# Kernel optimization log

Hardware: AMD Instinct MI355X
Metric: run time of the kernel (lower is better)

## Reference

```python
import jax, jax.numpy as jnp
import numpy as np

DIM = 512
HEADS = 8
DIM_HEAD = 64
BLOCKS = 6
EXCHANGES = 3
EPS = 1.1920929e-07  # torch.finfo(float32).eps used by RMSNorm(eps=None)


def _rmsnorm(x, w):
    return x * jax.lax.rsqrt(jnp.mean(x * x, axis=-1, keepdims=True) + EPS) * w


def _attention(x, ctx, nw, wq, wkv, wo):
    # x: [B, i, d] queries; ctx: [B, j, d] context (NOT normalized, as in original)
    B = x.shape[0]
    xn = _rmsnorm(x, nw)
    q = jnp.einsum('bid,ed->bie', xn, wq)
    kv = jnp.einsum('bjd,ed->bje', ctx, wkv)
    k, v = jnp.split(kv, 2, axis=-1)
    heads = lambda t: t.reshape(B, t.shape[1], HEADS, DIM_HEAD).transpose(0, 2, 1, 3)
    q, k, v = heads(q), heads(k), heads(v)
    sim = jnp.einsum('bhid,bhjd->bhij', q, k)  # NOTE: original never applies self.scale
    attn = jax.nn.softmax(sim, axis=-1)
    out = jnp.einsum('bhij,bhjd->bhid', attn, v)
    out = out.transpose(0, 2, 1, 3).reshape(B, -1, HEADS * DIM_HEAD)
    return jnp.einsum('bie,de->bid', out, wo)


def _feedforward(x, nw, kw, kb, vw, vb):
    q = _rmsnorm(x, nw)
    h = jnp.einsum('...d,ed->...e', q, kw) + kb
    sim, gates = jnp.split(h, 2, axis=-1)
    h = sim * jax.nn.gelu(gates, approximate=False)  # F.gelu default = exact erf
    return jnp.einsum('...e,de->...d', h, vw) + vb


def _forward(tokens, attn_norm_w, attn_wq, attn_wkv, attn_wo,
             ff_norm_w, ff_keys_w, ff_keys_b, ff_values_w, ff_values_b,
             res_norm_w, res_wq, res_wkv, res_wo):
    b, n, d = tokens.shape
    tokens = jnp.broadcast_to(tokens[None], (BLOCKS, b, n, d))
    messages = [tokens]
    for _ in range(EXCHANGES):
        flat = tokens.reshape(BLOCKS * b, n, d)
        attended = _attention(flat, flat, attn_norm_w, attn_wq, attn_wkv, attn_wo)
        attended = attended.reshape(BLOCKS, b, n, d)
        retrieved = _feedforward(tokens, ff_norm_w, ff_keys_w, ff_keys_b, ff_values_w, ff_values_b)
        messages += [attended, retrieved]
        packed = jnp.concatenate(messages, axis=0)           # [M, b, n, d]
        M = packed.shape[0]
        # einops: repeat 'm b n d -> (b blocks) n m d'
        ctx = jnp.broadcast_to(packed.transpose(1, 2, 0, 3)[:, None], (b, BLOCKS, n, M, d))
        ctx = ctx.reshape(b * BLOCKS * n, M, d)
        # queries packed '(blocks b) n d' then '* n d' -> [blocks*b*n, 1, d]
        q = tokens.reshape(BLOCKS * b * n, 1, d)
        pooled = _attention(q, ctx, res_norm_w, res_wq, res_wkv, res_wo)
        tokens = pooled.reshape(BLOCKS, b, n, d)
    return tokens


def setup_inputs() -> dict:
    key = jax.random.key(0)
    ks = jax.random.split(key, 12)
    b, n, d = 2, 256, DIM
    di = HEADS * DIM_HEAD
    dff = int(d * 4.0 * 2 / 3)
    s = lambda k, shp, fan: (jax.random.normal(k, shp, jnp.float32) / np.sqrt(fan)).astype(jnp.float32)
    return {
        'tokens': jax.random.normal(ks[0], (b, n, d), jnp.float32),
        'attn_norm_w': 1.0 + 0.05 * jax.random.normal(ks[1], (d,), jnp.float32),
        'attn_wq': s(ks[2], (di, d), d),
        'attn_wkv': s(ks[3], (2 * di, d), d),
        'attn_wo': s(ks[4], (d, di), di),
        'ff_norm_w': 1.0 + 0.05 * jax.random.normal(ks[5], (d,), jnp.float32),
        'ff_keys_w': s(ks[6], (2 * dff, d), d),
        'ff_keys_b': 0.01 * jax.random.normal(ks[7], (2 * dff,), jnp.float32),
        'ff_values_w': s(ks[8], (d, dff), dff),
        'ff_values_b': 0.01 * jax.random.normal(ks[9], (d,), jnp.float32),
        'res_norm_w': 1.0 + 0.05 * jax.random.normal(ks[10], (d,), jnp.float32),
        'res_wq': s(ks[11], (di, d), d),
        'res_wkv': s(jax.random.fold_in(key, 100), (2 * di, d), d),
        'res_wo': s(jax.random.fold_in(key, 101), (d, di), di),
    }


def reference(tokens, attn_norm_w, attn_wq, attn_wkv, attn_wo,
              ff_norm_w, ff_keys_w, ff_keys_b, ff_values_w, ff_values_b,
              res_norm_w, res_wq, res_wkv, res_wo):
    return _forward(tokens, attn_norm_w, attn_wq, attn_wkv, attn_wo,
                    ff_norm_w, ff_keys_w, ff_keys_b, ff_values_w, ff_values_b,
                    res_norm_w, res_wq, res_wkv, res_wo)
```

## Files before the change

### kernel.cpp

```cpp
#include <hip/hip_runtime.h>
#include <math.h>

#define Dm   512
#define Nn_  256
#define Bv   2
#define NTD  1024
#define NH   8
#define DH   64
#define DFF  1365
#define DFF2 2730
#define KFF  1408
#define NFF  2816
#define NMD  14
#define EPSR 1.1920929e-07f


typedef _Float16 h16;
typedef h16  v8h  __attribute__((ext_vector_type(8)));
typedef float v4f __attribute__((ext_vector_type(4)));

__device__ inline h16 f2h(float v) { return (h16)v; }

__device__ inline void glds16(const void* g, void* l) {
    __builtin_amdgcn_global_load_lds((const __attribute__((address_space(1))) void*)g,
                                     (__attribute__((address_space(3))) void*)l, 16, 0, 0);
}

struct GDesc {
    const h16* A;
    const h16* W;
    const float* bias;
    float* C;
    h16* Cbf;
    long Apl, Wpl, bfpl;
    int lda, ldw, ldc, Nd, mbase, K, mode, nbx;
};

template <int BM>
__global__ __launch_bounds__(256) void mega_gemm(GDesc d0, GDesc d1, GDesc d2,
                                                 int n0, int n01)
{
    constexpr int MI = BM / 32;
    constexpr int ASEG = BM / 16;
    constexpr int NSEG = 2 * ASEG + 16;
    constexpr int BUF = 2 * BM * 32 + 2 * 4096;
    constexpr int AH = 0, AL = BM * 32, WH = 2 * BM * 32, WL = 2 * BM * 32 + 4096;
    __shared__ h16 lds[2 * BUF];

    GDesc d; int lb = blockIdx.x;
    if (lb < n0) d = d0;
    else if (lb < n01) { d = d1; lb -= n0; }
    else { d = d2; lb -= n01; }
    const int bx = lb % d.nbx;
    const int by = lb / d.nbx;

    const int tid = threadIdx.x;
    const int wid = tid >> 6;
    const int lane = tid & 63;
    const int wm = wid >> 1, wn = wid & 1;
    const int row16 = lane & 15, quad = lane >> 4;
    const long i0 = (long)bx * BM;
    const long j0 = (long)by * 128;
    const int l4 = lane >> 2;
    const int l2s = ((lane & 3) ^ (l4 & 3)) * 8;
    const int ksw = (quad ^ (row16 & 3)) * 8;

    auto stage = [&](int k0, h16* buf) {
        #pragma unroll
        for (int s = 0; s < NSEG / 4; ++s) {
            const int sg = wid * (NSEG / 4) + s;
            const h16* src;
            int dst;
            if (sg < ASEG) {
                src = d.A + (i0 + sg * 16 + l4) * (long)d.lda + k0 + l2s;
                dst = AH + sg * 512;
            } else if (sg < 2 * ASEG) {
                const int r = sg - ASEG;
                src = d.A + d.Apl + (i0 + r * 16 + l4) * (long)d.lda + k0 + l2s;
                dst = AL + r * 512;
            } else if (sg < 2 * ASEG + 8) {
                const int r = sg - 2 * ASEG;
                src = d.W + (j0 + r * 16 + l4) * (long)d.ldw + k0 + l2s;
                dst = WH + r * 512;
            } else {
                const int r = sg - 2 * ASEG - 8;
                src = d.W + d.Wpl + (j0 + r * 16 + l4) * (long)d.ldw + k0 + l2s;
                dst = WL + r * 512;
            }
            glds16(src, &buf[dst]);
        }
    };

    v4f acc[MI][4];
    #pragma unroll
    for (int a = 0; a < MI; ++a)
        #pragma unroll
        for (int b = 0; b < 4; ++b) acc[a][b] = (v4f){0.f, 0.f, 0.f, 0.f};

    stage(0, lds);
    int cur = 0;
    for (int k0 = 0; k0 < d.K; k0 += 32) {
        __syncthreads();
        h16* cbuf = &lds[cur * BUF];
        if (k0 + 32 < d.K) stage(k0 + 32, &lds[(cur ^ 1) * BUF]);

        v8h af[MI], al[MI];
        #pragma unroll
        for (int mi = 0; mi < MI; ++mi) {
            const int aoff = (wm * (BM / 2) + mi * 16 + row16) * 32 + ksw;
            af[mi] = *(const v8h*)&cbuf[AH + aoff];
            al[mi] = *(const v8h*)&cbuf[AL + aoff];
        }
        #pragma unroll
        for (int nj = 0; nj < 4; ++nj) {
            const int boff = (wn * 64 + nj * 16 + row16) * 32 + ksw;
            v8h bh = *(const v8h*)&cbuf[WH + boff];
            v8h bl = *(const v8h*)&cbuf[WL + boff];
            #pragma unroll
            for (int mi = 0; mi < MI; ++mi) {
                acc[mi][nj] = __builtin_amdgcn_mfma_f32_16x16x32_f16(af[mi], bh, acc[mi][nj], 0, 0, 0);
                acc[mi][nj] = __builtin_amdgcn_mfma_f32_16x16x32_f16(af[mi], bl, acc[mi][nj], 0, 0, 0);
                acc[mi][nj] = __builtin_amdgcn_mfma_f32_16x16x32_f16(al[mi], bh, acc[mi][nj], 0, 0, 0);
            }
        }
        cur ^= 1;
    }

    #pragma unroll
    for (int nj = 0; nj < 4; ++nj) {
        const int col = (int)j0 + wn * 64 + nj * 16 + row16;
        if (col < d.Nd) {
            const float bv = d.bias ? d.bias[col] : 0.f;
            #pragma unroll
            for (int mi = 0; mi < MI; ++mi) {
                #pragma unroll
                for (int r = 0; r < 4; ++r) {
                    const long row = i0 + wm * (BM / 2) + mi * 16 + quad * 4 + r;
                    const float v = acc[mi][nj][r] + bv;
                    if (d.mode == 0) {
                        d.C[row * (long)d.ldc + col] = v;
                    } else if (d.mode == 1) {
                        const long idx = row * (long)d.ldc + col;
                        const h16 hi = f2h(v);
                        d.Cbf[idx] = hi; d.Cbf[idx + d.bfpl] = f2h(v - (float)hi);
                    } else if (d.mode == 2) {
                        const long idx = row * (long)d.ldc + col;
                        d.C[idx] = v;
                        const h16 hi = f2h(v);
                        d.Cbf[idx] = hi; d.Cbf[idx + d.bfpl] = f2h(v - (float)hi);
                    } else if (d.mode == 3) {
                        const int srel = (int)(row >> 10);
                        const int rr = (int)row & 1023;
                        const int md = (d.mbase + srel) * 2 + (rr >> 9);
                        const long orow = (long)(((rr >> 8) & 1) * 256 + (rr & 255)) * NMD + md;
                        d.C[orow * 1024 + col] = v;
                    } else if (d.mode == 4) {
                        const h16 hi = f2h(v);
                        const h16 lo = f2h(v - (float)hi);
                        if (col < 512) {
                            const long idx = row * 512 + col;
                            d.Cbf[idx] = hi; d.Cbf[idx + d.bfpl] = lo;
                        } else {
                            const int c = col - 512;
                            const int bh_ = ((int)(row >> 8)) * 8 + (c >> 6);
                            const long idx = (((long)bh_ * 64 + (c & 63)) << 8) + (row & 255);
                            h16* vtp = (h16*)d.C;
                            vtp[idx] = hi; vtp[idx + d.bfpl] = lo;
                        }
                    } else {
                        const int g = (int)(row >> 9), bb = ((int)row >> 8) & 1, nn = (int)row & 255;
                        #pragma unroll
                        for (int rep = 0; rep < 3; ++rep) {
                            const long orow = (long)(((g * 3 + rep) * 2 + bb) * 256 + nn);
                            d.C[orow * (long)d.ldc + col] = v;
                        }
                    }
                }
            }
        }
    }
}

__global__ void cvt_hilo(const float* __restrict__ x, int Ms, int Ks, int Kp,
                         h16* __restrict__ y, long plane, int total)
{
    const int idx = blockIdx.x * 256 + threadIdx.x;
    if (idx >= total) return;
    const int row = idx / Kp;
    const int col = idx - row * Kp;
    const float v = (row < Ms && col < Ks) ? x[(long)row * Ks + col] : 0.f;
    const h16 hi = f2h(v);
    y[idx] = hi;
    y[idx + plane] = f2h(v - (float)hi);
}

__global__ __launch_bounds__(256) void rmsnorm3_bf(
    const float* __restrict__ x,
    const float* __restrict__ w0, const float* __restrict__ w1,
    const float* __restrict__ w2,
    h16* __restrict__ y0, h16* __restrict__ y1,
    h16* __restrict__ y2, long plane)
{
    const int r = blockIdx.x;
    const float* xr = x + (long)r * Dm;
    const int t = threadIdx.x;
    const float a = xr[t];
    const float b = xr[t + 256];
    float ss = a * a + b * b;
    #pragma unroll
    for (int off = 32; off > 0; off >>= 1) ss += __shfl_xor(ss, off, 64);
    __shared__ float w4[4];
    if ((t & 63) == 0) w4[t >> 6] = ss;
    __syncthreads();
    const float rs = rsqrtf((w4[0] + w4[1] + w4[2] + w4[3]) * (1.f / 512.f) + EPSR);
    const float na = a * rs, nb = b * rs;
    const long ia = (long)r * Dm + t, ib = ia + 256;
    h16 h;
    float v;
    v = na * w0[t];       h = f2h(v); y0[ia] = h; y0[ia + plane] = f2h(v - (float)h);
    v = nb * w0[t + 256]; h = f2h(v); y0[ib] = h; y0[ib + plane] = f2h(v - (float)h);
    v = na * w1[t];       h = f2h(v); y1[ia] = h; y1[ia + plane] = f2h(v - (float)h);
    v = nb * w1[t + 256]; h = f2h(v); y1[ib] = h; y1[ib + plane] = f2h(v - (float)h);
    v = na * w2[t];       h = f2h(v); y2[ia] = h; y2[ia + plane] = f2h(v - (float)h);
    v = nb * w2[t + 256]; h = f2h(v); y2[ib] = h; y2[ib + plane] = f2h(v - (float)h);
}

__global__ __launch_bounds__(256) void glu_gelu_bf(
    const float* __restrict__ h, h16* __restrict__ y, long plane)
{
    const int r = blockIdx.x;
    const float* row = h + (long)r * NFF;
    for (int c = threadIdx.x; c < KFF; c += 256) {
        float v = 0.f;
        if (c < DFF) {
            const float sim = row[c];
            const float g = row[c + DFF];
            v = sim * (0.5f * g * (1.f + erff(g * 0.70710678118654752440f)));
        }
        const long idx = (long)r * KFF + c;
        const h16 hi = f2h(v);
        y[idx] = hi;
        y[idx + plane] = f2h(v - (float)hi);
    }
}

__global__ __launch_bounds__(256) void attn_self_mfma(
    const h16* __restrict__ qhl, const h16* __restrict__ khl,
    const h16* __restrict__ vtb, long pl, h16* __restrict__ outbf)
{
    __shared__ h16 kh[4096], kl[4096], vh[4096], vl[4096];
    __shared__ h16 pH[4 * 1024], pL[4 * 1024];

    const int bat = blockIdx.x >> 5;
    const int head = (blockIdx.x >> 2) & 7;
    const int qc = blockIdx.x & 3;
    const int t = threadIdx.x;
    const int w = t >> 6, lane = t & 63;
    const int row16 = lane & 15, quad = lane >> 4;

    v8h qh[2], ql[2];
    {
        const long qrow = (long)bat * 256 + qc * 64 + w * 16 + row16;
        const h16* qp = qhl + qrow * 512 + head * 64 + quad * 8;
        qh[0] = *(const v8h*)qp;        qh[1] = *(const v8h*)(qp + 32);
        ql[0] = *(const v8h*)(qp + pl); ql[1] = *(const v8h*)(qp + pl + 32);
    }

    v4f O[4];
    #pragma unroll
    for (int i = 0; i < 4; ++i) O[i] = (v4f){0.f, 0.f, 0.f, 0.f};
    float m[4] = {-1e30f, -1e30f, -1e30f, -1e30f};
    float l[4] = {0.f, 0.f, 0.f, 0.f};

    const int sj = t >> 3;
    const int sc = t & 7;
    const long kbase = ((long)bat * 256) * 512 + head * 64;
    const long vbase = ((long)(bat * 8 + head) * 64) << 8;

    for (int jc = 0; jc < 256; jc += 64) {
        __syncthreads();
        #pragma unroll
        for (int rep = 0; rep < 2; ++rep) {
            const int row = sj + rep * 32;
            const int dsw = row * 64 + ((sc ^ (row & 7)) * 8);
            const h16* ks = khl + kbase + (long)(jc + row) * 512 + sc * 8;
            const h16* vs = vtb + vbase + ((long)row << 8) + jc + sc * 8;
            *(v8h*)&kh[dsw] = *(const v8h*)ks;
            *(v8h*)&kl[dsw] = *(const v8h*)(ks + pl);
            *(v8h*)&vh[dsw] = *(const v8h*)vs;
            *(v8h*)&vl[dsw] = *(const v8h*)(vs + pl);
        }
        __syncthreads();

        v4f S[4];
        #pragma unroll
        for (int i = 0; i < 4; ++i) S[i] = (v4f){0.f, 0.f, 0.f, 0.f};
        #pragma unroll
        for (int kk = 0; kk < 2; ++kk) {
            #pragma unroll
            for (int tile = 0; tile < 4; ++tile) {
                const int off = (tile * 16 + row16) * 64 + (((kk * 4 + quad) ^ (row16 & 7)) * 8);
                v8h bh = *(const v8h*)&kh[off];
                v8h bl = *(const v8h*)&kl[off];
                S[tile] = __builtin_amdgcn_mfma_f32_16x16x32_f16(qh[kk], bh, S[tile], 0, 0, 0);
                S[tile] = __builtin_amdgcn_mfma_f32_16x16x32_f16(qh[kk], bl, S[tile], 0, 0, 0);
                S[tile] = __builtin_amdgcn_mfma_f32_16x16x32_f16(ql[kk], bh, S[tile], 0, 0, 0);
            }
        }

        float mc[4], sums[4], alpha[4];
        #pragma unroll
        for (int r = 0; r < 4; ++r) {
            float v = fmaxf(fmaxf(S[0][r], S[1][r]), fmaxf(S[2][r], S[3][r]));
            v = fmaxf(v, __shfl_xor(v, 1, 64));
            v = fmaxf(v, __shfl_xor(v, 2, 64));
            v = fmaxf(v, __shfl_xor(v, 4, 64));
            v = fmaxf(v, __shfl_xor(v, 8, 64));
            mc[r] = v;
        }
        #pragma unroll
        for (int r = 0; r < 4; ++r) {
            const float mn = fmaxf(m[r], mc[r]);
            alpha[r] = __expf(m[r] - mn);
            m[r] = mn;
            sums[r] = 0.f;
        }
        #pragma unroll
        for (int tile = 0; tile < 4; ++tile) {
            #pragma unroll
            for (int r = 0; r < 4; ++r) {
                const float p = __expf(S[tile][r] - m[r]);
                S[tile][r] = p;
                sums[r] += p;
            }
        }
        #pragma unroll
        for (int r = 0; r < 4; ++r) {
            float v = sums[r];
            v += __shfl_xor(v, 1, 64);
            v += __shfl_xor(v, 2, 64);
            v += __shfl_xor(v, 4, 64);
            v += __shfl_xor(v, 8, 64);
            l[r] = l[r] * alpha[r] + v;
        }
        #pragma unroll
        for (int tile = 0; tile < 4; ++tile)
            #pragma unroll
            for (int r = 0; r < 4; ++r) O[tile][r] *= alpha[r];

        #pragma unroll
        for (int tile = 0; tile < 4; ++tile) {
            const int chunkcol = tile * 2 + (row16 >> 3);
            #pragma unroll
            for (int r = 0; r < 4; ++r) {
                const int prow = quad * 4 + r;
                const int addr = w * 1024 + prow * 64 +
                                 ((chunkcol ^ (prow & 7)) * 8) + (row16 & 7);
                const float p = S[tile][r];
                const h16 hi = f2h(p);
                pH[addr] = hi;
                pL[addr] = f2h(p - (float)hi);
            }
        }

        #pragma unroll
        for (int kk = 0; kk < 2; ++kk) {
            const int poff = w * 1024 + row16 * 64 + (((kk * 4 + quad) ^ (row16 & 7)) * 8);
            v8h pa = *(const v8h*)&pH[poff];
            v8h pb = *(const v8h*)&pL[poff];
            #pragma unroll
            for (int tile = 0; tile < 4; ++tile) {
                const int off = (tile * 16 + row16) * 64 + (((kk * 4 + quad) ^ (row16 & 7)) * 8);
                v8h vbh = *(const v8h*)&vh[off];
                v8h vbl = *(const v8h*)&vl[off];
                O[tile] = __builtin_amdgcn_mfma_f32_16x16x32_f16(pa, vbh, O[tile], 0, 0, 0);
                O[tile] = __builtin_amdgcn_mfma_f32_16x16x32_f16(pa, vbl, O[tile], 0, 0, 0);
                O[tile] = __builtin_amdgcn_mfma_f32_16x16x32_f16(pb, vbh, O[tile], 0, 0, 0);
            }
        }
    }

    #pragma unroll
    for (int tile = 0; tile < 4; ++tile) {
        const int dim = tile * 16 + row16;
        #pragma unroll
        for (int r = 0; r < 4; ++r) {
            const long grow = (long)bat * 256 + qc * 64 + w * 16 + quad * 4 + r;
            const float v = O[tile][r] / l[r];
            const long idx = grow * 512 + head * 64 + dim;
            const h16 hi = f2h(v);
            outbf[idx] = hi;
            outbf[idx + pl] = f2h(v - (float)hi);
        }
    }
}

template <int M>
__global__ __launch_bounds__(128) void attn_pool_kernel(
    const float* __restrict__ qb, const float* __restrict__ kvc3,
    h16* __restrict__ outbf, long plane)
{
    const int rb = blockIdx.x >> 3;
    const int h = blockIdx.x & 7;
    __shared__ float k_lds[M * 66];
    __shared__ float v_lds[M * 66];
    __shared__ float q_lds[2 * 64];
    __shared__ float p_lds[2 * 64];
    const int t = threadIdx.x;
    const int g = rb >> 8, nn = rb & 255;

    for (int idx = t; idx < M * 64; idx += 128) {
        const int m = idx >> 6, d = idx & 63;
        const long base = ((long)rb * NMD + m) * 1024 + h * DH + d;
        k_lds[m * 66 + d] = kvc3[base];
        v_lds[m * 66 + d] = kvc3[base + 512];
    }
    {
        const int w = t >> 6, dd = t & 63;
        const long iq = (long)(g * 2 + w) * 256 + nn;
        q_lds[t] = qb[iq * Dm + h * DH + dd];
    }
    __syncthreads();

    const int w = t >> 6;
    const int lane = t & 63;
    float s = -1e30f;
    if (lane < M) {
        s = 0.f;
        const float* kr = &k_lds[lane * 66];
        const float* qr = &q_lds[w * 64];
        #pragma unroll
        for (int dd = 0; dd < 64; dd += 2) {
            s = fmaf(qr[dd], kr[dd], s);
            s = fmaf(qr[dd + 1], kr[dd + 1], s);
        }
    }
    float mx = s;
    #pragma unroll
    for (int off = 32; off > 0; off >>= 1) mx = fmaxf(mx, __shfl_xor(mx, off, 64));
    const float p = __expf(s - mx);
    float l = p;
    #pragma unroll
    for (int off = 32; off > 0; off >>= 1) l += __shfl_xor(l, off, 64);
    p_lds[w * 64 + lane] = p / l;

    float o = 0.f;
    const float* pr = &p_lds[w * 64];
    #pragma unroll
    for (int m = 0; m < M; ++m)
        o = fmaf(pr[m], v_lds[m * 66 + lane], o);

    const long iq = (long)(g * 2 + w) * 256 + nn;
    const long oidx = iq * Dm + h * DH + lane;
    const h16 hi = f2h(o);
    outbf[oidx] = hi;
    outbf[oidx + plane] = f2h(o - (float)hi);
}

__global__ void replicate_kernel(const float* __restrict__ src,
                                 float* __restrict__ tokens,
                                 h16* __restrict__ tokbf, long tpl,
                                 h16* __restrict__ msg0, long mpl)
{
    const int idx = blockIdx.x * blockDim.x + threadIdx.x;
    if (idx >= NTD * Dm) return;
    const float v = src[idx & (Bv * Nn_ * Dm - 1)];
    tokens[idx] = v;
    const h16 hi = f2h(v);
    const h16 lo = f2h(v - (float)hi);
    tokbf[idx] = hi; tokbf[idx + tpl] = lo;
    msg0[idx] = hi; msg0[idx + mpl] = lo;
}

extern "C" void kernel_launch(void* const* d_in, const int* in_sizes, int n_in,
                              void* d_out, int out_size, void* d_ws, size_t ws_size,
                              hipStream_t stream)
{
    const float* tok_in       = (const float*)d_in[0];
    const float* attn_norm_w  = (const float*)d_in[1];
    const float* attn_wq      = (const float*)d_in[2];
    const float* attn_wkv     = (const float*)d_in[3];
    const float* attn_wo      = (const float*)d_in[4];
    const float* ff_norm_w    = (const float*)d_in[5];
    const float* ff_keys_w    = (const float*)d_in[6];
    const float* ff_keys_b    = (const float*)d_in[7];
    const float* ff_values_w  = (const float*)d_in[8];
    const float* ff_values_b  = (const float*)d_in[9];
    const float* res_norm_w   = (const float*)d_in[10];
    const float* res_wq       = (const float*)d_in[11];
    const float* res_wkv      = (const float*)d_in[12];
    const float* res_wo       = (const float*)d_in[13];

    float* ws = (float*)d_ws;
    float* kvc3   = ws;
    float* tokens = kvc3 + 512L * NMD * 1024;
    float* qbuf   = tokens + (long)NTD * Dm;
    float* hbuf   = qbuf + (long)NTD * Dm;

    h16* us = (h16*)(hbuf + (long)NTD * NFF);
    const long apl = (long)NTD * Dm;
    const long mpl = 7L * NTD * Dm;
    const long hpl = (long)NTD * KFF;
    const long vtpl = (long)NTD * Dm;
    const long w1 = 512L * 512, w2 = 1024L * 512, w3 = (long)NFF * 512, w4 = 512L * KFF;
    h16* msgs_bf = us; us += 2 * mpl;
    h16* tokbf   = us; us += 2 * apl;
    h16* xa      = us; us += 2 * apl;
    h16* xf      = us; us += 2 * apl;
    h16* xr      = us; us += 2 * apl;
    h16* abf     = us; us += 2 * apl;
    h16* hbf     = us; us += 2 * hpl;
    h16* qhl     = us; us += 2 * apl;
    h16* khl     = us; us += 2 * apl;
    h16* vtb     = us; us += 2 * vtpl;
    h16* wqb  = us; us += 2 * w1;
    h16* wkvb = us; us += 2 * w2;
    h16* wob  = us; us += 2 * w1;
    h16* fkb  = us; us += 2 * w3;
    h16* fvb  = us; us += 2 * w4;
    h16* rqb  = us; us += 2 * w1;
    h16* rkvb = us; us += 2 * w2;
    h16* rob  = us; us += 2 * w1;

    auto cvtw = [&](const float* src, int Ms, int Ks, int Kp, int Mpad,
                    h16* dst, long pl) {
        const int tot = Mpad * Kp;
        cvt_hilo<<<(tot + 255) / 256, 256, 0, stream>>>(src, Ms, Ks, Kp, dst, pl, tot);
    };
    cvtw(attn_wq,     512,  512,  512, 512,  wqb,  w1);
    cvtw(attn_wkv,    1024, 512,  512, 1024, wkvb, w2);
    cvtw(attn_wo,     512,  512,  512, 512,  wob,  w1);
    cvtw(ff_keys_w,   DFF2, 512,  512, NFF,  fkb,  w3);
    cvtw(ff_values_w, 512,  DFF,  KFF, 512,  fvb,  w4);
    cvtw(res_wq,      512,  512,  512, 512,  rqb,  w1);
    cvtw(res_wkv,    1024,  512,  512, 1024, rkvb, w2);
    cvtw(res_wo,      512,  512,  512, 512,  rob,  w1);

    replicate_kernel<<<(NTD * Dm + 255) / 256, 256, 0, stream>>>(
        tok_in, tokens, tokbf, apl, msgs_bf, mpl);

    auto mk = [](const h16* A, long Apl, int lda,
                 const h16* W, long Wpl, int ldw,
                 const float* bias, float* C, int ldc, int Nd,
                 h16* Cbf, long bfpl, int mbase, int K,
                 int mode, int nbx) -> GDesc {
        GDesc d;
        d.A = A; d.Apl = Apl; d.lda = lda;
        d.W = W; d.Wpl = Wpl; d.ldw = ldw;
        d.bias = bias; d.C = C; d.ldc = ldc; d.Nd = Nd;
        d.Cbf = Cbf; d.bfpl = bfpl; d.mbase = mbase; d.K = K;
        d.mode = mode; d.nbx = nbx;
        return d;
    };

    for (int e = 0; e < 3; ++e) {
        rmsnorm3_bf<<<NTD, 256, 0, stream>>>(tokens, attn_norm_w, ff_norm_w, res_norm_w,
                                             xa, xf, xr, apl);
        {
            GDesc dwq  = mk(xa,    apl, 512, wqb,  w1, 512, nullptr,   nullptr, 512, 512,
                            qhl, apl, 0, 512, 1, 16);
            GDesc dwkv = mk(tokbf, apl, 512, wkvb, w2, 512, nullptr,   (float*)vtb, 1024, 1024,
                            khl, apl, 0, 512, 4, 16);
            GDesc dffk = mk(xf,    apl, 512, fkb,  w3, 512, ff_keys_b, hbuf,  NFF,  DFF2,
                            nullptr, 0, 0, 512, 0, 16);
            mega_gemm<64><<<544, 256, 0, stream>>>(dwq, dwkv, dffk, 64, 192);
        }
        attn_self_mfma<<<4 * NH * 4, 256, 0, stream>>>(qhl, khl, vtb, apl, abf);
        glu_gelu_bf<<<NTD, 256, 0, stream>>>(hbuf, hbf, hpl);
        {
            GDesc dwo  = mk(abf, apl, 512,  wob, w1, 512,  nullptr,     nullptr, 512, 512,
                            msgs_bf + (1 + 2 * e) * (long)NTD * Dm, mpl, 0, 512, 1, 16);
            GDesc dffv = mk(hbf, hpl, KFF,  fvb, w4, KFF,  ff_values_b, nullptr, 512, 512,
                            msgs_bf + (2 + 2 * e) * (long)NTD * Dm, mpl, 0, KFF, 1, 16);
            GDesc drq  = mk(xr, apl, 512, rqb, w1, 512, nullptr, qbuf, 512, 512,
                            nullptr, 0, 0, 512, 0, 16);
            mega_gemm<64><<<192, 256, 0, stream>>>(dwo, dffv, drq, 64, 128);
        }
        {
            const int s0 = (e == 0) ? 0 : (1 + 2 * e);
            const int ns = (e == 0) ? 3 : 2;
            GDesc drkv = mk(msgs_bf + (long)s0 * NTD * Dm, mpl, 512, rkvb, w2, 512,
                            nullptr, kvc3, 1024, 1024, nullptr, 0, s0, 512, 3, ns * 16);
            const int nb = ns * 16 * 8;
            mega_gemm<64><<<nb, 256, 0, stream>>>(drkv, drkv, drkv, nb, nb);
        }
        if (e == 0)      attn_pool_kernel<6><<<512 * NH, 128, 0, stream>>>(qbuf, kvc3, abf, apl);
        else if (e == 1) attn_pool_kernel<10><<<512 * NH, 128, 0, stream>>>(qbuf, kvc3, abf, apl);
        else             attn_pool_kernel<14><<<512 * NH, 128, 0, stream>>>(qbuf, kvc3, abf, apl);
        {
            if (e < 2) {
                GDesc dro = mk(abf, apl, 512, rob, w1, 512, nullptr, tokens, 512, 512,
                               tokbf, apl, 0, 512, 2, 16);
                mega_gemm<64><<<64, 256, 0, stream>>>(dro, dro, dro, 64, 64);
            } else {
                GDesc dro = mk(abf, apl, 512, rob, w1, 512, nullptr, (float*)d_out, 512, 512,
                               nullptr, 0, 0, 512, 5, 16);
                mega_gemm<64><<<64, 256, 0, stream>>>(dro, dro, dro, 64, 64);
            }
        }
    }
}
```

Baseline: 522.4 us.

## Fold output projections into residual KV weights and fuse attention with GLU

Precomputes the products of res_wkv with attn_wo and ff_values_w, plus a folded bias, once per call. The KV projections of the attended and retrieved messages can then be computed straight from the attention output and the GLU activations, which drops the message hi/lo buffers and the separate KV GEMM launch. The self-attention and GLU-GELU kernels are merged into one launch, mega_gemm takes a fourth descriptor so more GEMMs share a launch, and the final projection uses BM=32 tiles for more blocks. In exchange there is a per-call weight-folding GEMM, a larger inner K (1408) on the FFN path, and an extra rounding step from the precomposed weights.

```diff
diff --git a/kernel.cpp b/kernel.cpp
--- a/kernel.cpp
+++ b/kernel.cpp
@@ -14,7 +14,6 @@
 #define NMD  14
 #define EPSR 1.1920929e-07f
 
-
 typedef _Float16 h16;
 typedef h16  v8h  __attribute__((ext_vector_type(8)));
 typedef float v4f __attribute__((ext_vector_type(4)));
@@ -37,8 +36,8 @@
 };
 
 template <int BM>
-__global__ __launch_bounds__(256) void mega_gemm(GDesc d0, GDesc d1, GDesc d2,
-                                                 int n0, int n01)
+__global__ __launch_bounds__(256) void mega_gemm(GDesc d0, GDesc d1, GDesc d2, GDesc d3,
+                                                 int n0, int n01, int n012)
 {
     constexpr int MI = BM / 32;
     constexpr int ASEG = BM / 16;
@@ -50,7 +49,8 @@
     GDesc d; int lb = blockIdx.x;
     if (lb < n0) d = d0;
     else if (lb < n01) { d = d1; lb -= n0; }
-    else { d = d2; lb -= n01; }
+    else if (lb < n012) { d = d2; lb -= n01; }
+    else { d = d3; lb -= n012; }
     const int bx = lb % d.nbx;
     const int by = lb / d.nbx;
 
@@ -149,9 +149,8 @@
                         const h16 hi = f2h(v);
                         d.Cbf[idx] = hi; d.Cbf[idx + d.bfpl] = f2h(v - (float)hi);
                     } else if (d.mode == 3) {
-                        const int srel = (int)(row >> 10);
                         const int rr = (int)row & 1023;
-                        const int md = (d.mbase + srel) * 2 + (rr >> 9);
+                        const int md = d.mbase * 2 + (rr >> 9);
                         const long orow = (long)(((rr >> 8) & 1) * 256 + (rr & 255)) * NMD + md;
                         d.C[orow * 1024 + col] = v;
                     } else if (d.mode == 4) {
@@ -194,6 +193,30 @@
     y[idx + plane] = f2h(v - (float)hi);
 }
 
+__global__ void cvt_hilo_T(const float* __restrict__ x, int R, int C,
+                           h16* __restrict__ y, long plane, int total)
+{
+    const int idx = blockIdx.x * 256 + threadIdx.x;
+    if (idx >= total) return;
+    const int row = idx / R;
+    const int col = idx - row * R;
+    const float v = (row < C) ? x[(long)col * C + row] : 0.f;
+    const h16 hi = f2h(v);
+    y[idx] = hi;
+    y[idx + plane] = f2h(v - (float)hi);
+}
+
+__global__ void fold_bias(const float* __restrict__ wkv, const float* __restrict__ b,
+                          float* __restrict__ out)
+{
+    const int n = blockIdx.x * 256 + threadIdx.x;
+    if (n >= 1024) return;
+    float s = 0.f;
+    const float* row = wkv + (long)n * 512;
+    for (int d2 = 0; d2 < 512; ++d2) s = fmaf(row[d2], b[d2], s);
+    out[n] = s;
+}
+
 __global__ __launch_bounds__(256) void rmsnorm3_bf(
     const float* __restrict__ x,
     const float* __restrict__ w0, const float* __restrict__ w1,
@@ -225,29 +248,29 @@
     v = nb * w2[t + 256]; h = f2h(v); y2[ib] = h; y2[ib + plane] = f2h(v - (float)h);
 }
 
-__global__ __launch_bounds__(256) void glu_gelu_bf(
-    const float* __restrict__ h, h16* __restrict__ y, long plane)
-{
-    const int r = blockIdx.x;
-    const float* row = h + (long)r * NFF;
-    for (int c = threadIdx.x; c < KFF; c += 256) {
-        float v = 0.f;
-        if (c < DFF) {
-            const float sim = row[c];
-            const float g = row[c + DFF];
-            v = sim * (0.5f * g * (1.f + erff(g * 0.70710678118654752440f)));
-        }
-        const long idx = (long)r * KFF + c;
-        const h16 hi = f2h(v);
-        y[idx] = hi;
-        y[idx + plane] = f2h(v - (float)hi);
-    }
-}
-
-__global__ __launch_bounds__(256) void attn_self_mfma(
+__global__ __launch_bounds__(256) void attn_glu(
     const h16* __restrict__ qhl, const h16* __restrict__ khl,
-    const h16* __restrict__ vtb, long pl, h16* __restrict__ outbf)
-{
+    const h16* __restrict__ vtb, long pl, h16* __restrict__ outbf,
+    const float* __restrict__ hbuf, h16* __restrict__ hbf, long hpl)
+{
+    if (blockIdx.x >= 128) {
+        const int r = blockIdx.x - 128;
+        const float* row = hbuf + (long)r * NFF;
+        for (int c = threadIdx.x; c < KFF; c += 256) {
+            float v = 0.f;
+            if (c < DFF) {
+                const float sim = row[c];
+                const float g = row[c + DFF];
+                v = sim * (0.5f * g * (1.f + erff(g * 0.70710678118654752440f)));
+            }
+            const long idx = (long)r * KFF + c;
+            const h16 hi = f2h(v);
+            hbf[idx] = hi;
+            hbf[idx + hpl] = f2h(v - (float)hi);
+        }
+        return;
+    }
+
     __shared__ h16 kh[4096], kl[4096], vh[4096], vl[4096];
     __shared__ h16 pH[4 * 1024], pL[4 * 1024];
 
@@ -459,17 +482,15 @@
 
 __global__ void replicate_kernel(const float* __restrict__ src,
                                  float* __restrict__ tokens,
-                                 h16* __restrict__ tokbf, long tpl,
-                                 h16* __restrict__ msg0, long mpl)
+                                 h16* __restrict__ tokbf, long tpl)
 {
     const int idx = blockIdx.x * blockDim.x + threadIdx.x;
     if (idx >= NTD * Dm) return;
     const float v = src[idx & (Bv * Nn_ * Dm - 1)];
     tokens[idx] = v;
     const h16 hi = f2h(v);
-    const h16 lo = f2h(v - (float)hi);
-    tokbf[idx] = hi; tokbf[idx + tpl] = lo;
-    msg0[idx] = hi; msg0[idx + mpl] = lo;
+    tokbf[idx] = hi;
+    tokbf[idx + tpl] = f2h(v - (float)hi);
 }
 
 extern "C" void kernel_launch(void* const* d_in, const int* in_sizes, int n_in,
@@ -496,48 +517,50 @@
     float* tokens = kvc3 + 512L * NMD * 1024;
     float* qbuf   = tokens + (long)NTD * Dm;
     float* hbuf   = qbuf + (long)NTD * Dm;
-
-    h16* us = (h16*)(hbuf + (long)NTD * NFF);
+    float* biasWf = hbuf + (long)NTD * NFF;
+
+    h16* us = (h16*)(biasWf + 1024);
     const long apl = (long)NTD * Dm;
-    const long mpl = 7L * NTD * Dm;
     const long hpl = (long)NTD * KFF;
     const long vtpl = (long)NTD * Dm;
-    const long w1 = 512L * 512, w2 = 1024L * 512, w3 = (long)NFF * 512, w4 = 512L * KFF;
-    h16* msgs_bf = us; us += 2 * mpl;
-    h16* tokbf   = us; us += 2 * apl;
-    h16* xa      = us; us += 2 * apl;
-    h16* xf      = us; us += 2 * apl;
-    h16* xr      = us; us += 2 * apl;
-    h16* abf     = us; us += 2 * apl;
-    h16* hbf     = us; us += 2 * hpl;
-    h16* qhl     = us; us += 2 * apl;
-    h16* khl     = us; us += 2 * apl;
-    h16* vtb     = us; us += 2 * vtpl;
-    h16* wqb  = us; us += 2 * w1;
-    h16* wkvb = us; us += 2 * w2;
-    h16* wob  = us; us += 2 * w1;
-    h16* fkb  = us; us += 2 * w3;
-    h16* fvb  = us; us += 2 * w4;
-    h16* rqb  = us; us += 2 * w1;
-    h16* rkvb = us; us += 2 * w2;
-    h16* rob  = us; us += 2 * w1;
+    const long w1 = 512L * 512, w2 = 1024L * 512, w3 = (long)NFF * 512;
+    const long w5 = (long)KFF * 512;
+    const long wa_pl = 1024L * 512;
+    const long wf_pl = 1024L * KFF;
+    h16* tokbf = us; us += 2 * apl;
+    h16* xa    = us; us += 2 * apl;
+    h16* xf    = us; us += 2 * apl;
+    h16* xr    = us; us += 2 * apl;
+    h16* abf   = us; us += 2 * apl;
+    h16* hbf   = us; us += 2 * hpl;
+    h16* qhl   = us; us += 2 * apl;
+    h16* khl   = us; us += 2 * apl;
+    h16* vtb   = us; us += 2 * vtpl;
+    h16* wqb   = us; us += 2 * w1;
+    h16* wkvb  = us; us += 2 * w2;
+    h16* fkb   = us; us += 2 * w3;
+    h16* rqb   = us; us += 2 * w1;
+    h16* rkvb  = us; us += 2 * w2;
+    h16* rob   = us; us += 2 * w1;
+    h16* woTb  = us; us += 2 * w1;
+    h16* fvwTb = us; us += 2 * w5;
+    h16* Wab   = us; us += 2 * wa_pl;
+    h16* Wfb   = us; us += 2 * wf_pl;
 
     auto cvtw = [&](const float* src, int Ms, int Ks, int Kp, int Mpad,
                     h16* dst, long pl) {
         const int tot = Mpad * Kp;
         cvt_hilo<<<(tot + 255) / 256, 256, 0, stream>>>(src, Ms, Ks, Kp, dst, pl, tot);
     };
-    cvtw(attn_wq,     512,  512,  512, 512,  wqb,  w1);
-    cvtw(attn_wkv,    1024, 512,  512, 1024, wkvb, w2);
-    cvtw(attn_wo,     512,  512,  512, 512,  wob,  w1);
-    cvtw(ff_keys_w,   DFF2, 512,  512, NFF,  fkb,  w3);
-    cvtw(ff_values_w, 512,  DFF,  KFF, 512,  fvb,  w4);
-    cvtw(res_wq,      512,  512,  512, 512,  rqb,  w1);
-    cvtw(res_wkv,    1024,  512,  512, 1024, rkvb, w2);
-    cvtw(res_wo,      512,  512,  512, 512,  rob,  w1);
-
-    replicate_kernel<<<(NTD * Dm + 255) / 256, 256, 0, stream>>>(
-        tok_in, tokens, tokbf, apl, msgs_bf, mpl);
+    cvtw(attn_wq,   512,  512, 512, 512,  wqb,  w1);
+    cvtw(attn_wkv,  1024, 512, 512, 1024, wkvb, w2);
+    cvtw(ff_keys_w, DFF2, 512, 512, NFF,  fkb,  w3);
+    cvtw(res_wq,    512,  512, 512, 512,  rqb,  w1);
+    cvtw(res_wkv,   1024, 512, 512, 1024, rkvb, w2);
+    cvtw(res_wo,    512,  512, 512, 512,  rob,  w1);
+    cvt_hilo_T<<<(512 * 512 + 255) / 256, 256, 0, stream>>>(attn_wo, 512, 512, woTb, w1, 512 * 512);
+    cvt_hilo_T<<<((int)w5 + 255) / 256, 256, 0, stream>>>(ff_values_w, 512, DFF, fvwTb, w5, (int)w5);
+    fold_bias<<<4, 256, 0, stream>>>(res_wkv, ff_values_b, biasWf);
 
     auto mk = [](const h16* A, long Apl, int lda,
                  const h16* W, long Wpl, int ldw,
@@ -553,36 +576,43 @@
         return d;
     };
 
+    {
+        GDesc dWf = mk(rkvb, w2, 512, fvwTb, w5, 512, nullptr, nullptr, KFF, KFF,
+                       Wfb, wf_pl, 0, 512, 1, 16);
+        GDesc dWa = mk(rkvb, w2, 512, woTb, w1, 512, nullptr, nullptr, 512, 512,
+                       Wab, wa_pl, 0, 512, 1, 16);
+        mega_gemm<64><<<240, 256, 0, stream>>>(dWf, dWa, dWa, dWa, 176, 240, 240);
+    }
+
+    replicate_kernel<<<(NTD * Dm + 255) / 256, 256, 0, stream>>>(tok_in, tokens, tokbf, apl);
+
     for (int e = 0; e < 3; ++e) {
         rmsnorm3_bf<<<NTD, 256, 0, stream>>>(tokens, attn_norm_w, ff_norm_w, res_norm_w,
                                              xa, xf, xr, apl);
         {
-            GDesc dwq  = mk(xa,    apl, 512, wqb,  w1, 512, nullptr,   nullptr, 512, 512,
+            GDesc dffk = mk(xf,    apl, 512, fkb,  w3, 512, ff_keys_b, hbuf, NFF, DFF2,
+                            nullptr, 0, 0, 512, 0, 16);
+            GDesc dwkv = mk(tokbf, apl, 512, wkvb, w2, 512, nullptr, (float*)vtb, 1024, 1024,
+                            khl, apl, 0, 512, 4, 16);
+            GDesc dwq  = mk(xa,    apl, 512, wqb,  w1, 512, nullptr, nullptr, 512, 512,
                             qhl, apl, 0, 512, 1, 16);
-            GDesc dwkv = mk(tokbf, apl, 512, wkvb, w2, 512, nullptr,   (float*)vtb, 1024, 1024,
-                            khl, apl, 0, 512, 4, 16);
-            GDesc dffk = mk(xf,    apl, 512, fkb,  w3, 512, ff_keys_b, hbuf,  NFF,  DFF2,
-                            nullptr, 0, 0, 512, 0, 16);
-            mega_gemm<64><<<544, 256, 0, stream>>>(dwq, dwkv, dffk, 64, 192);
-        }
-        attn_self_mfma<<<4 * NH * 4, 256, 0, stream>>>(qhl, khl, vtb, apl, abf);
-        glu_gelu_bf<<<NTD, 256, 0, stream>>>(hbuf, hbf, hpl);
+            mega_gemm<64><<<544, 256, 0, stream>>>(dffk, dwkv, dwq, dwq, 352, 480, 544);
+        }
+        attn_glu<<<1152, 256, 0, stream>>>(qhl, khl, vtb, apl, abf, hbuf, hbf, hpl);
         {
-            GDesc dwo  = mk(abf, apl, 512,  wob, w1, 512,  nullptr,     nullptr, 512, 512,
-                            msgs_bf + (1 + 2 * e) * (long)NTD * Dm, mpl, 0, 512, 1, 16);
-            GDesc dffv = mk(hbf, hpl, KFF,  fvb, w4, KFF,  ff_values_b, nullptr, 512, 512,
-                            msgs_bf + (2 + 2 * e) * (long)NTD * Dm, mpl, 0, KFF, 1, 16);
-            GDesc drq  = mk(xr, apl, 512, rqb, w1, 512, nullptr, qbuf, 512, 512,
-                            nullptr, 0, 0, 512, 0, 16);
-            mega_gemm<64><<<192, 256, 0, stream>>>(dwo, dffv, drq, 64, 128);
-        }
-        {
-            const int s0 = (e == 0) ? 0 : (1 + 2 * e);
-            const int ns = (e == 0) ? 3 : 2;
-            GDesc drkv = mk(msgs_bf + (long)s0 * NTD * Dm, mpl, 512, rkvb, w2, 512,
-                            nullptr, kvc3, 1024, 1024, nullptr, 0, s0, 512, 3, ns * 16);
-            const int nb = ns * 16 * 8;
-            mega_gemm<64><<<nb, 256, 0, stream>>>(drkv, drkv, drkv, nb, nb);
+            GDesc dffvKV = mk(hbf, hpl, KFF, Wfb, wf_pl, KFF, biasWf, kvc3, 1024, 1024,
+                              nullptr, 0, 2 + 2 * e, KFF, 3, 16);
+            GDesc dwoKV  = mk(abf, apl, 512, Wab, wa_pl, 512, nullptr, kvc3, 1024, 1024,
+                              nullptr, 0, 1 + 2 * e, 512, 3, 16);
+            GDesc drq    = mk(xr, apl, 512, rqb, w1, 512, nullptr, qbuf, 512, 512,
+                              nullptr, 0, 0, 512, 0, 16);
+            if (e == 0) {
+                GDesc dtokKV = mk(tokbf, apl, 512, rkvb, w2, 512, nullptr, kvc3, 1024, 1024,
+                                  nullptr, 0, 0, 512, 3, 16);
+                mega_gemm<64><<<448, 256, 0, stream>>>(dffvKV, dwoKV, drq, dtokKV, 128, 256, 320);
+            } else {
+                mega_gemm<64><<<320, 256, 0, stream>>>(dffvKV, dwoKV, drq, drq, 128, 256, 320);
+            }
         }
         if (e == 0)      attn_pool_kernel<6><<<512 * NH, 128, 0, stream>>>(qbuf, kvc3, abf, apl);
         else if (e == 1) attn_pool_kernel<10><<<512 * NH, 128, 0, stream>>>(qbuf, kvc3, abf, apl);
@@ -590,13 +620,13 @@
         {
             if (e < 2) {
                 GDesc dro = mk(abf, apl, 512, rob, w1, 512, nullptr, tokens, 512, 512,
-                               tokbf, apl, 0, 512, 2, 16);
-                mega_gemm<64><<<64, 256, 0, stream>>>(dro, dro, dro, 64, 64);
+                               tokbf, apl, 0, 512, 2, 32);
+                mega_gemm<32><<<128, 256, 0, stream>>>(dro, dro, dro, dro, 128, 128, 128);
             } else {
                 GDesc dro = mk(abf, apl, 512, rob, w1, 512, nullptr, (float*)d_out, 512, 512,
-                               nullptr, 0, 0, 512, 5, 16);
-                mega_gemm<64><<<64, 256, 0, stream>>>(dro, dro, dro, 64, 64);
-            }
-        }
-    }
-}
+                               nullptr, 0, 0, 512, 5, 32);
+                mega_gemm<32><<<128, 256, 0, stream>>>(dro, dro, dro, dro, 128, 128, 128);
+            }
+        }
+    }
+}
```

New measurement: 490.4 us. 6.1% less time.
